# Performance work log

Measured on AMD Instinct MI355X. Metric: run time of the kernel, lower is better.

The kernel has to match this reference:

```python
import jax, jax.numpy as jnp
import numpy as np

S = 100                     # MC weight samples
B = 128                     # batch
CONV1 = (100, 20, 1, 5, 5)  # (S, Cout, Cin, kh, kw)
CONV2 = (100, 50, 20, 5, 5)
AFF1 = (100, 500, 800)      # (S, out, in)
AFF2 = (100, 10, 500)
W_OFF = np.cumsum([0, 500, 25000, 400000, 5000])
B_OFF = np.cumsum([0, 20, 50, 500, 10])
NW, NB = 430500, 580


def _softplus(r):
    return jnp.log1p(jnp.exp(r))  # sigma_T(rho) = log(1 + exp(rho))


def _conv(h, w, b):
    # h: (B, S or 1, Cin, H, W); w: (S, Cout, Cin, kh, kw); b: (S, Cout)
    def one(xs, ws):  # xs: (B,Cin,H,W), ws: (Cout,Cin,kh,kw)
        return jax.lax.conv_general_dilated(xs, ws, (1, 1), 'VALID')
    if h.shape[1] == 1:  # shared input broadcast over samples (first layer)
        out = jax.vmap(one, in_axes=(None, 0), out_axes=1)(h[:, 0], w)
    else:
        out = jax.vmap(one, in_axes=(1, 0), out_axes=1)(h, w)
    return out + b[None, :, :, None, None]  # (B,S,Cout,H',W')


def _maxpool(h):  # 2x2 stride-2 over trailing spatial dims
    return jax.lax.reduce_window(h, -jnp.inf, jax.lax.max,
                                 (1, 1, 1, 2, 2), (1, 1, 1, 2, 2), 'VALID')


def setup_inputs() -> dict:
    key = jax.random.key(0)
    ks = jax.random.split(key, 4)
    x = jax.random.normal(ks[0], (B, 1, 28, 28), dtype=jnp.float32)
    e = jax.random.normal(ks[1], (S, NW + NB), dtype=jnp.float32)
    mu_w = jax.random.normal(ks[2], (NW,), dtype=jnp.float32) * 0.05
    rho_w = jnp.ones((NW,), dtype=jnp.float32) * 0.5
    mu_b = jax.random.normal(ks[3], (NB,), dtype=jnp.float32) * 0.05
    rho_b = jnp.ones((NB,), dtype=jnp.float32) * 0.5
    return {"x": x, "e": e, "mu_w": mu_w, "rho_w": rho_w,
            "mu_b": mu_b, "rho_b": rho_b}


def reference(x, e, mu_w, rho_w, mu_b, rho_b):
    # reparameterized per-sample weights: (S, NW) and (S, NB)
    w = mu_w + _softplus(rho_w) * e[:, :NW]
    b = mu_b + _softplus(rho_b) * e[:, NW:]

    h = x[:, None]  # (B,1,1,28,28): singleton MC dim broadcasts
    # conv1 + relu + pool
    h = _conv(h, w[:, W_OFF[0]:W_OFF[1]].reshape(CONV1), b[:, B_OFF[0]:B_OFF[1]])
    h = _maxpool(jax.nn.relu(h))                     # (B,S,20,12,12)
    # conv2 + relu + pool
    h = _conv(h, w[:, W_OFF[1]:W_OFF[2]].reshape(CONV2), b[:, B_OFF[1]:B_OFF[2]])
    h = _maxpool(jax.nn.relu(h))                     # (B,S,50,4,4)
    h = h.reshape(h.shape[0], h.shape[1], -1)        # (B,S,800)
    # aff1 + relu
    w3 = w[:, W_OFF[2]:W_OFF[3]].reshape(AFF1)
    h = jax.nn.relu(jnp.einsum('bsi,soi->bso', h, w3) + b[None, :, B_OFF[2]:B_OFF[3]])
    # aff2 + log_softmax
    w4 = w[:, W_OFF[3]:W_OFF[4]].reshape(AFF2)
    h = jnp.einsum('bsi,soi->bso', h, w4) + b[None, :, B_OFF[3]:B_OFF[4]]
    h = jax.nn.log_softmax(h, axis=-1)               # (B,S,10)
    return h.mean(axis=1)                            # eval path: mean over MC samples
```

## Files before the change

kernel.cpp:

```cpp
#include <hip/hip_runtime.h>
#include <math.h>

#define Sn 100
#define Bn 128
#define NWc 430500
#define EWc 431080

typedef __attribute__((ext_vector_type(8)))  short bhalf8;
typedef __attribute__((ext_vector_type(16))) float fx16;

__device__ __forceinline__ float sp_f(float r){
    return fmaxf(r, 0.f) + log1pf(__expf(-fabsf(r)));
}
__device__ __forceinline__ ushort bfr(float f){
    union { float f; uint u; } c; c.f = f;
    uint r = (c.u + 0x7FFFu + ((c.u >> 16) & 1u)) >> 16;
    return (ushort)r;
}

__global__ void k00_sp(const float* __restrict__ rho_w, const float* __restrict__ rho_b,
                       float* __restrict__ sp_all){
    int i = blockIdx.x * blockDim.x + threadIdx.x;
    if (i < NWc)      sp_all[i] = sp_f(rho_w[i]);
    else if (i < EWc) sp_all[i] = sp_f(rho_b[i - NWc]);
}

__global__ __launch_bounds__(256) void k0_w3t(const float* __restrict__ e,
        const float* __restrict__ mu_w, const float* __restrict__ sp_all,
        ushort* __restrict__ w3){
    __shared__ __align__(16) ushort ls[2][20*808];
    int oc = blockIdx.x;
    int sp = blockIdx.y;
    int s0 = sp * 2;
    int o0 = oc * 20;
    int tid = threadIdx.x;
    const float* e0 = e + (size_t)s0*EWc + 25500 + (size_t)o0*800;
    const float* e1 = e0 + EWc;
    const float* mb = mu_w   + 25500 + (size_t)o0*800;
    const float* pb = sp_all + 25500 + (size_t)o0*800;
    #pragma unroll 2
    for (int j = tid; j < 4000; j += 256){
        int o = j / 200, k4 = j - o*200;
        float4 mv = *(const float4*)(mb + j*4);
        float4 sv = *(const float4*)(pb + j*4);
        float4 ev0 = *(const float4*)(e0 + j*4);
        float4 ev1 = *(const float4*)(e1 + j*4);
        ushort4 t0, t1;
        t0.x = bfr(fmaf(sv.x, ev0.x, mv.x));
        t0.y = bfr(fmaf(sv.y, ev0.y, mv.y));
        t0.z = bfr(fmaf(sv.z, ev0.z, mv.z));
        t0.w = bfr(fmaf(sv.w, ev0.w, mv.w));
        t1.x = bfr(fmaf(sv.x, ev1.x, mv.x));
        t1.y = bfr(fmaf(sv.y, ev1.y, mv.y));
        t1.z = bfr(fmaf(sv.z, ev1.z, mv.z));
        t1.w = bfr(fmaf(sv.w, ev1.w, mv.w));
        *(ushort4*)&ls[0][o*808 + k4*4] = t0;
        *(ushort4*)&ls[1][o*808 + k4*4] = t1;
    }
    __syncthreads();
    if (tid < 200){
        int kt = tid >> 3, l8 = tid & 7;
        #pragma unroll
        for (int ss = 0; ss < 2; ++ss){
            ushort* wb = w3 + (size_t)(s0 + ss)*400000 + kt*16000 + o0*32;
            #pragma unroll
            for (int it = 0; it < 10; ++it){
                int idx = it*8 + l8;
                int o = idx >> 2, kp = (idx & 3)*8;
                uint4 v = *(const uint4*)&ls[ss][o*808 + kt*32 + kp];
                *(uint4*)(wb + idx*8) = v;
            }
        }
    }
}

__global__ void k0_small(const float* __restrict__ e, const float* __restrict__ mu_w,
                       const float* __restrict__ sp_all, const float* __restrict__ mu_b,
                       float* __restrict__ w1, ushort* __restrict__ w2r,
                       float* __restrict__ w4, float* __restrict__ ball){
    const int per = 31080;
    int idx = blockIdx.x * blockDim.x + threadIdx.x;
    if (idx >= Sn * per) return;
    int s = idx / per, j = idx % per;
    if (j < 500){
        float v = fmaf(sp_all[j], e[(size_t)s*EWc + j], mu_w[j]);
        w1[s*500 + j] = v;
    } else if (j < 25500){
        int g = j;
        float v = fmaf(sp_all[g], e[(size_t)s*EWc + g], mu_w[g]);
        int j2 = j - 500;
        int oc = j2 / 500, rem = j2 % 500;
        int ic = rem / 25, kk = rem % 25;
        w2r[(size_t)s*51200 + (kk*64 + oc)*32 + ic] = bfr(v);
    } else if (j < 30500){
        int g = 425500 + (j - 25500);
        float v = fmaf(sp_all[g], e[(size_t)s*EWc + g], mu_w[g]);
        w4[s*5000 + (j - 25500)] = v;
    } else {
        int k = j - 30500;
        float v = fmaf(sp_all[NWc + k], e[(size_t)s*EWc + NWc + k], mu_b[k]);
        ball[s*580 + k] = v;
    }
}

__global__ __launch_bounds__(256, 2) void k1_conv1(const float* __restrict__ x,
        const float* __restrict__ w1, const float* __restrict__ ball,
        ushort* __restrict__ h1p){
    __shared__ __align__(16) float xs[784];
    __shared__ __align__(16) float w1s[500];
    __shared__ float b1s[20];
    __shared__ __align__(16) ushort ots[2880];
    int bid = blockIdx.x;
    int s = bid / Bn, b = bid % Bn;
    int tid = threadIdx.x;
    for (int i = tid; i < 784; i += 256) xs[i] = x[b*784 + i];
    for (int i = tid; i < 500; i += 256) w1s[i] = w1[s*500 + i];
    if (tid < 20) b1s[tid] = ball[s*580 + tid];
    __syncthreads();
    if (tid < 240){
        int c = tid / 12, y = tid % 12;

        float acc0[24], acc1[24];
        #pragma unroll
        for (int i = 0; i < 24; ++i){ acc0[i] = 0.f; acc1[i] = 0.f; }

        #pragma unroll
        for (int ky = 0; ky < 5; ++ky){
            float rlo[28], rhi[28];
            const float* plo = &xs[(2*y + ky) * 28];
            const float* phi = &xs[(2*y + ky + 1) * 28];
            #pragma unroll
            for (int cc = 0; cc < 28; cc += 4){
                float4 v0 = *(const float4*)(plo + cc);
                rlo[cc] = v0.x; rlo[cc+1] = v0.y; rlo[cc+2] = v0.z; rlo[cc+3] = v0.w;
                float4 v1 = *(const float4*)(phi + cc);
                rhi[cc] = v1.x; rhi[cc+1] = v1.y; rhi[cc+2] = v1.z; rhi[cc+3] = v1.w;
            }
            #pragma unroll
            for (int kx = 0; kx < 5; ++kx){
                float wv = w1s[c*25 + ky*5 + kx];
                #pragma unroll
                for (int cx = 0; cx < 24; ++cx){
                    acc0[cx] = fmaf(rlo[cx + kx], wv, acc0[cx]);
                    acc1[cx] = fmaf(rhi[cx + kx], wv, acc1[cx]);
                }
            }
        }
        float bias = b1s[c];
        #pragma unroll
        for (int px = 0; px < 12; ++px){
            float m = fmaxf(fmaxf(acc0[2*px], acc0[2*px+1]),
                            fmaxf(acc1[2*px], acc1[2*px+1]));
            ots[(y*12 + px)*20 + c] = bfr(fmaxf(m + bias, 0.f));
        }
    }
    __syncthreads();
    const uint* o32 = (const uint*)ots;
    uint* g32 = (uint*)(h1p + (s*Bn + b)*2880);
    for (int j = tid; j < 1440; j += 256) g32[j] = o32[j];
}

__global__ __launch_bounds__(256, 4) void k2_direct(const ushort* __restrict__ h1p,
        const ushort* __restrict__ w2r, const float* __restrict__ ball,
        ushort* __restrict__ h2p){
    __shared__ __align__(16) ushort img[4*4608];
    int bid = blockIdx.x;
    int s = bid >> 5, g = bid & 31;
    int tid = threadIdx.x;
    const uint* g32 = (const uint*)(h1p + (size_t)(s*Bn + g*4)*2880);
    uint* l32 = (uint*)img;
    for (int j = tid; j < 5760; j += 256){
        int im = j / 1440, r = j - im*1440;
        int p = r / 10, u = r - p*10;
        l32[im*2304 + ((p*16 + u) ^ ((p & 7) << 2))] = g32[j];
    }
    for (int j = tid; j < 3456; j += 256){
        int im = j / 864, r = j - im*864;
        int p = r / 6, u = 10 + (r - p*6);
        l32[im*2304 + ((p*16 + u) ^ ((p & 7) << 2))] = 0u;
    }
    __syncthreads();

    int wv = tid >> 6, l = tid & 63;
    int l31 = l & 31, q = l >> 5;
    const ushort* imgw = img + wv*4608;
    int pixb0 = ((l31      ) >> 3)*12 + (l31 & 7);
    int pixb1 = ((l31 + 32 ) >> 3)*12 + (l31 & 7);
    const ushort* wb0 = w2r + (size_t)(s*25)*2048 + (l31     )*32 + q*8;
    const ushort* wb1 = w2r + (size_t)(s*25)*2048 + (l31 + 32)*32 + q*8;
    fx16 acc00 = (fx16)0.f, acc01 = (fx16)0.f, acc10 = (fx16)0.f, acc11 = (fx16)0.f;

    bhalf8 b0c = *(const bhalf8*)(wb0);
    bhalf8 b1c = *(const bhalf8*)(wb1);
    bhalf8 b2c = *(const bhalf8*)(wb0 + 16);
    bhalf8 b3c = *(const bhalf8*)(wb1 + 16);

    #pragma unroll 1
    for (int kk = 0; kk < 25; ++kk){
        int kn = (kk < 24) ? (kk + 1) : 24;
        bhalf8 b0n = *(const bhalf8*)(wb0 + kn*2048);
        bhalf8 b1n = *(const bhalf8*)(wb1 + kn*2048);
        bhalf8 b2n = *(const bhalf8*)(wb0 + kn*2048 + 16);
        bhalf8 b3n = *(const bhalf8*)(wb1 + kn*2048 + 16);

        int ky = kk / 5, kx = kk - ky*5;
        int poff = ky*12 + kx;
        int p0 = pixb0 + poff, p1 = pixb1 + poff;
        int sw0 = (p0 & 7) << 3, sw1 = (p1 & 7) << 3;

        bhalf8 a00 = *(const bhalf8*)(imgw + ((p0*32 +      q*8) ^ sw0));
        bhalf8 a10 = *(const bhalf8*)(imgw + ((p1*32 +      q*8) ^ sw1));
        acc00 = __builtin_amdgcn_mfma_f32_32x32x16_bf16(a00, b0c, acc00, 0, 0, 0);
        acc01 = __builtin_amdgcn_mfma_f32_32x32x16_bf16(a00, b1c, acc01, 0, 0, 0);
        acc10 = __builtin_amdgcn_mfma_f32_32x32x16_bf16(a10, b0c, acc10, 0, 0, 0);
        acc11 = __builtin_amdgcn_mfma_f32_32x32x16_bf16(a10, b1c, acc11, 0, 0, 0);

        bhalf8 a01 = *(const bhalf8*)(imgw + ((p0*32 + 16 + q*8) ^ sw0));
        bhalf8 a11 = *(const bhalf8*)(imgw + ((p1*32 + 16 + q*8) ^ sw1));
        acc00 = __builtin_amdgcn_mfma_f32_32x32x16_bf16(a01, b2c, acc00, 0, 0, 0);
        acc01 = __builtin_amdgcn_mfma_f32_32x32x16_bf16(a01, b3c, acc01, 0, 0, 0);
        acc10 = __builtin_amdgcn_mfma_f32_32x32x16_bf16(a11, b2c, acc10, 0, 0, 0);
        acc11 = __builtin_amdgcn_mfma_f32_32x32x16_bf16(a11, b3c, acc11, 0, 0, 0);

        b0c = b0n; b1c = b1n; b2c = b2n; b3c = b3n;
    }
    int b = g*4 + wv;
    ushort* dst = h2p + (size_t)s*102400 + (size_t)b*32;
    #pragma unroll
    for (int nt = 0; nt < 2; ++nt){
        int oc = nt*32 + l31;
        if (oc >= 50) continue;
        float bias = ball[s*580 + 20 + oc];
        #pragma unroll
        for (int mt = 0; mt < 2; ++mt){
            fx16 a;
            if (nt == 0) a = mt ? acc10 : acc00;
            else         a = mt ? acc11 : acc01;
            #pragma unroll
            for (int gp = 0; gp < 2; ++gp){
                float p0 = fmaxf(fmaxf(a[8*gp+0], a[8*gp+1]), fmaxf(a[8*gp+4], a[8*gp+5]));
                float p1 = fmaxf(fmaxf(a[8*gp+2], a[8*gp+3]), fmaxf(a[8*gp+6], a[8*gp+7]));
                p0 = fmaxf(p0 + bias, 0.f);
                p1 = fmaxf(p1 + bias, 0.f);
                int py = mt*2 + gp;
                int i  = oc*16 + py*4 + 2*q;
                uint pk = (uint)bfr(p0) | ((uint)bfr(p1) << 16);
                *(uint*)(dst + (i >> 5)*4096 + (i & 31)) = pk;
            }
        }
    }
}

#define ICS 40
__global__ __launch_bounds__(256) void k3_mfma(const ushort* __restrict__ h2p,
        const ushort* __restrict__ w3, const float* __restrict__ ball,
        float* __restrict__ h3){
    __shared__ __align__(16) ushort As[128*ICS];
    __shared__ __align__(16) ushort Bsh[64*ICS];
    int bid = blockIdx.x;
    int s = bid >> 3, nblk = bid & 7;
    int o0 = nblk * 64;
    int tid = threadIdx.x;
    int wv = tid >> 6, l = tid & 63, l31 = l & 31, q = l >> 5;
    int wm = wv >> 1, wn = wv & 1;
    fx16 acc0 = (fx16)0.f, acc1 = (fx16)0.f;
    int rr = tid >> 2, rk = (tid & 3)*8;
    const ushort* Abase = h2p + (size_t)s*102400;
    const ushort* Bbase = w3  + (size_t)s*400000 + (size_t)o0*32;
    bool bvalid = (o0 + rr) < 500;
    const uint4 z4 = make_uint4(0u,0u,0u,0u);

    uint4 ar0, ar1, br;
    ar0 = *(const uint4*)(Abase + rr*32 + rk);
    ar1 = *(const uint4*)(Abase + (rr + 64)*32 + rk);
    br  = bvalid ? *(const uint4*)(Bbase + rr*32 + rk) : z4;

    for (int kt = 0; kt < 25; ++kt){
        __syncthreads();
        *(uint4*)&As[rr*ICS + rk]        = ar0;
        *(uint4*)&As[(rr + 64)*ICS + rk] = ar1;
        *(uint4*)&Bsh[rr*ICS + rk]       = br;
        __syncthreads();
        if (kt < 24){
            ar0 = *(const uint4*)(Abase + (kt+1)*4096 + rr*32 + rk);
            ar1 = *(const uint4*)(Abase + (kt+1)*4096 + (rr + 64)*32 + rk);
            br  = bvalid ? *(const uint4*)(Bbase + (kt+1)*16000 + rr*32 + rk) : z4;
        }
        #pragma unroll
        for (int ks = 0; ks < 2; ++ks){
            bhalf8 a0 = *(const bhalf8*)&As[(wm*64      + l31)*ICS + ks*16 + q*8];
            bhalf8 a1 = *(const bhalf8*)&As[(wm*64 + 32 + l31)*ICS + ks*16 + q*8];
            bhalf8 bb = *(const bhalf8*)&Bsh[(wn*32 + l31)*ICS + ks*16 + q*8];
            acc0 = __builtin_amdgcn_mfma_f32_32x32x16_bf16(a0, bb, acc0, 0, 0, 0);
            acc1 = __builtin_amdgcn_mfma_f32_32x32x16_bf16(a1, bb, acc1, 0, 0, 0);
        }
    }
    int o = o0 + wn*32 + l31;
    if (o < 500){
        float bias = ball[s*580 + 70 + o];
        #pragma unroll
        for (int mt = 0; mt < 2; ++mt){
            fx16 a = mt ? acc1 : acc0;
            #pragma unroll
            for (int reg = 0; reg < 16; ++reg){
                int row = (reg & 3) + 8*(reg >> 2) + 4*q;
                int b = wm*64 + mt*32 + row;
                h3[(size_t)(s*Bn + b)*500 + o] = fmaxf(a[reg] + bias, 0.f);
            }
        }
    }
}

__global__ __launch_bounds__(256) void k4a(const float* __restrict__ h3,
        const float* __restrict__ w4, const float* __restrict__ ball,
        float* __restrict__ lsw){
    int wv = threadIdx.x >> 6, lane = threadIdx.x & 63;
    int p = blockIdx.x*4 + wv;
    int s = p / Bn;
    const float* hp = &h3[(size_t)p*500];
    const float* wp = &w4[(size_t)s*5000];
    float part[10];
    #pragma unroll
    for (int o = 0; o < 10; ++o) part[o] = 0.f;
    for (int i = lane; i < 500; i += 64){
        float hv = hp[i];
        #pragma unroll
        for (int o = 0; o < 10; ++o)
            part[o] = fmaf(hv, wp[o*500 + i], part[o]);
    }
    #pragma unroll
    for (int o = 0; o < 10; ++o){
        #pragma unroll
        for (int d = 1; d < 64; d <<= 1)
            part[o] += __shfl_xor(part[o], d);
    }
    float v[10]; float m = -INFINITY;
    #pragma unroll
    for (int o = 0; o < 10; ++o){
        v[o] = part[o] + ball[s*580 + 570 + o];
        m = fmaxf(m, v[o]);
    }
    float sum = 0.f;
    #pragma unroll
    for (int o = 0; o < 10; ++o) sum += __expf(v[o] - m);
    float lse = m + __logf(sum);
    if (lane == 0){
        #pragma unroll
        for (int o = 0; o < 10; ++o) lsw[p*10 + o] = v[o] - lse;
    }
}

__global__ void k4b(const float* __restrict__ lsw, float* __restrict__ outp){
    int j = blockIdx.x * blockDim.x + threadIdx.x;
    if (j >= Bn*10) return;
    int b = j / 10, o = j % 10;
    float acc = 0.f;
    for (int s2 = 0; s2 < Sn; ++s2) acc += lsw[(s2*Bn + b)*10 + o];
    outp[j] = acc * (1.f / (float)Sn);
}

extern "C" void kernel_launch(void* const* d_in, const int* in_sizes, int n_in,
                              void* d_out, int out_size, void* d_ws, size_t ws_size,
                              hipStream_t stream){
    const float* x     = (const float*)d_in[0];
    const float* e     = (const float*)d_in[1];
    const float* mu_w  = (const float*)d_in[2];
    const float* rho_w = (const float*)d_in[3];
    const float* mu_b  = (const float*)d_in[4];
    const float* rho_b = (const float*)d_in[5];
    float* ws   = (float*)d_ws;
    float* w1     = ws;
    float* w4     = w1 + 50000;
    float* ball   = w4 + 500000;
    float* h3     = ball + 58000;
    float* lsw    = h3 + 6400000;
    float* sp_all = lsw + 128000;
    ushort* h1p = (ushort*)(sp_all + 431080);
    ushort* h2p = h1p + 36864000;
    ushort* w2r = h2p + 10240000;
    ushort* w3  = w2r + 5120000;
    float* outp = (float*)d_out;

    hipMemsetAsync(w2r, 0, (size_t)Sn*51200*2, stream);
    k00_sp   <<<(EWc + 255)/256, 256, 0, stream>>>(rho_w, rho_b, sp_all);
    k0_w3t   <<<dim3(25, 50), 256, 0, stream>>>(e, mu_w, sp_all, w3);
    k0_small <<<(Sn*31080 + 255)/256, 256, 0, stream>>>(e, mu_w, sp_all, mu_b, w1, w2r, w4, ball);
    k1_conv1 <<<Sn*Bn, 256, 0, stream>>>(x, w1, ball, h1p);
    k2_direct<<<Sn*32, 256, 0, stream>>>(h1p, w2r, ball, h2p);
    k3_mfma  <<<Sn*8, 256, 0, stream>>>(h2p, w3, ball, h3);
    k4a      <<<3200, 256, 0, stream>>>(h3, w4, ball, lsw);
    k4b      <<<(Bn*10 + 255)/256, 256, 0, stream>>>(lsw, outp);
}
```

Baseline: 543.1 us.

## Stage conv2 weight tiles through shared memory instead of per-wave global loads

Each block now loads the per-tap conv2 weight slice once cooperatively (one uint4 per thread) into a shared buffer, instead of every wave reading the same weights from global memory. Waves then read their B fragments from LDS, with a register prefetch of the next tap. This cuts redundant global/L2 traffic by a factor of four. In exchange it adds two block-wide barriers per tap iteration and extra LDS reads, which can stall the MFMA pipeline.

Result: faster. 526.8 us (-3.0%).

```diff
diff --git a/kernel.cpp b/kernel.cpp
--- a/kernel.cpp
+++ b/kernel.cpp
@@ -164,6 +164,7 @@
         const ushort* __restrict__ w2r, const float* __restrict__ ball,
         ushort* __restrict__ h2p){
     __shared__ __align__(16) ushort img[4*4608];
+    __shared__ __align__(16) ushort Bls[2048];
     int bid = blockIdx.x;
     int s = bid >> 5, g = bid & 31;
     int tid = threadIdx.x;
@@ -179,29 +180,27 @@
         int p = r / 6, u = 10 + (r - p*6);
         l32[im*2304 + ((p*16 + u) ^ ((p & 7) << 2))] = 0u;
     }
-    __syncthreads();
+
+    int oc_w = tid >> 2, c_w = tid & 3;
+    int P = ((c_w >> 1)*2 + (oc_w >> 5))*64 + (c_w & 1)*32 + (oc_w & 31);
+    uint4* bdst = (uint4*)&Bls[P*8];
+    const uint4* bsrc = (const uint4*)(w2r + (size_t)(s*25)*2048) + tid;
+    uint4 breg = bsrc[0];
 
     int wv = tid >> 6, l = tid & 63;
     int l31 = l & 31, q = l >> 5;
     const ushort* imgw = img + wv*4608;
     int pixb0 = ((l31      ) >> 3)*12 + (l31 & 7);
     int pixb1 = ((l31 + 32 ) >> 3)*12 + (l31 & 7);
-    const ushort* wb0 = w2r + (size_t)(s*25)*2048 + (l31     )*32 + q*8;
-    const ushort* wb1 = w2r + (size_t)(s*25)*2048 + (l31 + 32)*32 + q*8;
+    int lam = q*32 + l31;
     fx16 acc00 = (fx16)0.f, acc01 = (fx16)0.f, acc10 = (fx16)0.f, acc11 = (fx16)0.f;
 
-    bhalf8 b0c = *(const bhalf8*)(wb0);
-    bhalf8 b1c = *(const bhalf8*)(wb1);
-    bhalf8 b2c = *(const bhalf8*)(wb0 + 16);
-    bhalf8 b3c = *(const bhalf8*)(wb1 + 16);
+    *bdst = breg;
+    __syncthreads();
 
     #pragma unroll 1
     for (int kk = 0; kk < 25; ++kk){
-        int kn = (kk < 24) ? (kk + 1) : 24;
-        bhalf8 b0n = *(const bhalf8*)(wb0 + kn*2048);
-        bhalf8 b1n = *(const bhalf8*)(wb1 + kn*2048);
-        bhalf8 b2n = *(const bhalf8*)(wb0 + kn*2048 + 16);
-        bhalf8 b3n = *(const bhalf8*)(wb1 + kn*2048 + 16);
+        if (kk < 24) breg = bsrc[(kk + 1)*256];
 
         int ky = kk / 5, kx = kk - ky*5;
         int poff = ky*12 + kx;
@@ -210,19 +209,27 @@
 
         bhalf8 a00 = *(const bhalf8*)(imgw + ((p0*32 +      q*8) ^ sw0));
         bhalf8 a10 = *(const bhalf8*)(imgw + ((p1*32 +      q*8) ^ sw1));
-        acc00 = __builtin_amdgcn_mfma_f32_32x32x16_bf16(a00, b0c, acc00, 0, 0, 0);
-        acc01 = __builtin_amdgcn_mfma_f32_32x32x16_bf16(a00, b1c, acc01, 0, 0, 0);
-        acc10 = __builtin_amdgcn_mfma_f32_32x32x16_bf16(a10, b0c, acc10, 0, 0, 0);
-        acc11 = __builtin_amdgcn_mfma_f32_32x32x16_bf16(a10, b1c, acc11, 0, 0, 0);
-
         bhalf8 a01 = *(const bhalf8*)(imgw + ((p0*32 + 16 + q*8) ^ sw0));
         bhalf8 a11 = *(const bhalf8*)(imgw + ((p1*32 + 16 + q*8) ^ sw1));
-        acc00 = __builtin_amdgcn_mfma_f32_32x32x16_bf16(a01, b2c, acc00, 0, 0, 0);
-        acc01 = __builtin_amdgcn_mfma_f32_32x32x16_bf16(a01, b3c, acc01, 0, 0, 0);
-        acc10 = __builtin_amdgcn_mfma_f32_32x32x16_bf16(a11, b2c, acc10, 0, 0, 0);
-        acc11 = __builtin_amdgcn_mfma_f32_32x32x16_bf16(a11, b3c, acc11, 0, 0, 0);
-
-        b0c = b0n; b1c = b1n; b2c = b2n; b3c = b3n;
+        bhalf8 b0  = *(const bhalf8*)&Bls[       lam*8];
+        bhalf8 b1  = *(const bhalf8*)&Bls[ 512 + lam*8];
+        bhalf8 b2  = *(const bhalf8*)&Bls[1024 + lam*8];
+        bhalf8 b3  = *(const bhalf8*)&Bls[1536 + lam*8];
+
+        acc00 = __builtin_amdgcn_mfma_f32_32x32x16_bf16(a00, b0, acc00, 0, 0, 0);
+        acc01 = __builtin_amdgcn_mfma_f32_32x32x16_bf16(a00, b1, acc01, 0, 0, 0);
+        acc10 = __builtin_amdgcn_mfma_f32_32x32x16_bf16(a10, b0, acc10, 0, 0, 0);
+        acc11 = __builtin_amdgcn_mfma_f32_32x32x16_bf16(a10, b1, acc11, 0, 0, 0);
+        acc00 = __builtin_amdgcn_mfma_f32_32x32x16_bf16(a01, b2, acc00, 0, 0, 0);
+        acc01 = __builtin_amdgcn_mfma_f32_32x32x16_bf16(a01, b3, acc01, 0, 0, 0);
+        acc10 = __builtin_amdgcn_mfma_f32_32x32x16_bf16(a11, b2, acc10, 0, 0, 0);
+        acc11 = __builtin_amdgcn_mfma_f32_32x32x16_bf16(a11, b3, acc11, 0, 0, 0);
+
+        if (kk < 24){
+            __syncthreads();
+            *bdst = breg;
+            __syncthreads();
+        }
     }
     int b = g*4 + wv;
     ushort* dst = h2p + (size_t)s*102400 + (size_t)b*32;
```
